# Kernel tuning notes

Hardware: AMD Instinct MI355X
Metric: run time of the kernel (lower is better)

## Reference

```python
import jax, jax.numpy as jnp
import numpy as np

ORIG_H, ORIG_W = 256, 192
NUM_HEADS = 8
KSZ, SIGMA = 5, 2.0

def _gauss_kernel(dtype):
    off = jnp.arange(KSZ, dtype=jnp.float32) - (KSZ // 2)
    g = jnp.exp(-(off[:, None] ** 2 + off[None, :] ** 2) / (2.0 * SIGMA ** 2))
    return (g / g.sum()).astype(dtype)

def _gauss_pool(fm, kpts):
    # fm: (B,C,H,W), kpts: (B,N,2) [x,y] in original image coords -> (B,N,C)
    B, C, H, W = fm.shape
    scale = jnp.array([W / ORIG_W, H / ORIG_H], dtype=fm.dtype)
    rk = kpts * scale  # resized to feature-map coords
    off = jnp.arange(KSZ) - KSZ // 2
    ix = jnp.clip(jnp.round(rk[..., 0]).astype(jnp.int32)[..., None] + off, 0, W - 1)  # (B,N,K)
    iy = jnp.clip(jnp.round(rk[..., 1]).astype(jnp.int32)[..., None] + off, 0, H - 1)  # (B,N,K)
    fmT = fm.transpose(0, 2, 3, 1)  # (B,H,W,C)
    gather = jax.vmap(lambda f, yy, xx: f[yy[:, :, None], xx[:, None, :]])(fmT, iy, ix)  # (B,N,K,K,C)
    return jnp.einsum('bnyxc,yx->bnc', gather, _gauss_kernel(fm.dtype))

def _ln(x, g, b):
    m = x.mean(-1, keepdims=True)
    v = x.var(-1, keepdims=True)
    return (x - m) / jnp.sqrt(v + 1e-5) * g + b

def _gated_attn(x, wqkv, bqkv, wg, bg, wo, bo):
    # x: (M,S,C); headwise-gated multi-head self-attention
    M, S, C = x.shape
    H = NUM_HEADS
    d = C // H
    q, k, v = jnp.split(x @ wqkv + bqkv, 3, axis=-1)
    q = q.reshape(M, S, H, d); k = k.reshape(M, S, H, d); v = v.reshape(M, S, H, d)
    att = jax.nn.softmax(jnp.einsum('mshd,mthd->mhst', q, k) * (1.0 / np.sqrt(d)), axis=-1)
    o = jnp.einsum('mhst,mthd->mshd', att, v)
    gate = jax.nn.sigmoid(x @ wg + bg)  # (M,S,H) headwise gate
    o = (o * gate[..., None]).reshape(M, S, C)
    return o @ wo + bo

def _fuse(kf, ms, proj_p, attn_p):
    B, N, C = kf.shape
    meta = jnp.broadcast_to(ms[None], (B, N, C))
    w1, b1, g, beta, w2, b2 = proj_p
    h = _ln(jnp.concatenate([kf, meta], axis=-1) @ w1 + b1, g, beta)
    projected = jax.nn.relu(h) @ w2 + b2
    stacked = jnp.stack([kf, meta], axis=2).reshape(B * N, 2, C)  # (B*N,2,C)
    attended = _gated_attn(stacked, *attn_p).reshape(B, N, 2, C)
    return attended.mean(axis=2) + projected

def setup_inputs() -> dict:
    key = jax.random.key(0)
    ks = iter(jax.random.split(key, 48))
    B, N = 32, 17
    dims = [256, 512]
    inp = {}
    inp['fm0'] = jax.random.normal(next(ks), (B, 256, 96, 72), jnp.float32)
    inp['fm1'] = jax.random.normal(next(ks), (B, 512, 48, 36), jnp.float32)
    u = jax.random.uniform(next(ks), (B, N, 2), jnp.float32)
    inp['keypoints'] = u * jnp.array([ORIG_W - 1.0, ORIG_H - 1.0], jnp.float32)
    for i, C in enumerate(dims):
        s = 1.0 / np.sqrt(C)
        inp[f'ms{i}'] = jax.random.normal(next(ks), (N, C), jnp.float32) * s
        inp[f'p{i}_w1'] = jax.random.normal(next(ks), (2 * C, C), jnp.float32) * (1.0 / np.sqrt(2 * C))
        inp[f'p{i}_b1'] = jnp.zeros((C,), jnp.float32)
        inp[f'p{i}_g'] = jnp.ones((C,), jnp.float32)
        inp[f'p{i}_beta'] = jnp.zeros((C,), jnp.float32)
        inp[f'p{i}_w2'] = jax.random.normal(next(ks), (C, C), jnp.float32) * s
        inp[f'p{i}_b2'] = jnp.zeros((C,), jnp.float32)
        inp[f'a{i}_wqkv'] = jax.random.normal(next(ks), (C, 3 * C), jnp.float32) * s
        inp[f'a{i}_bqkv'] = jnp.zeros((3 * C,), jnp.float32)
        inp[f'a{i}_wg'] = jax.random.normal(next(ks), (C, NUM_HEADS), jnp.float32) * s
        inp[f'a{i}_bg'] = jnp.zeros((NUM_HEADS,), jnp.float32)
        inp[f'a{i}_wo'] = jax.random.normal(next(ks), (C, C), jnp.float32) * s
        inp[f'a{i}_bo'] = jnp.zeros((C,), jnp.float32)
    return inp

def reference(fm0, fm1, keypoints,
              ms0, p0_w1, p0_b1, p0_g, p0_beta, p0_w2, p0_b2,
              a0_wqkv, a0_bqkv, a0_wg, a0_bg, a0_wo, a0_bo,
              ms1, p1_w1, p1_b1, p1_g, p1_beta, p1_w2, p1_b2,
              a1_wqkv, a1_bqkv, a1_wg, a1_bg, a1_wo, a1_bo):
    kf0 = _gauss_pool(fm0, keypoints)
    f0 = _fuse(kf0, ms0, (p0_w1, p0_b1, p0_g, p0_beta, p0_w2, p0_b2),
               (a0_wqkv, a0_bqkv, a0_wg, a0_bg, a0_wo, a0_bo))
    kf1 = _gauss_pool(fm1, keypoints)
    f1 = _fuse(kf1, ms1, (p1_w1, p1_b1, p1_g, p1_beta, p1_w2, p1_b2),
               (a1_wqkv, a1_bqkv, a1_wg, a1_bg, a1_wo, a1_bo))
    return (f0, f1)
```

## Files before the change

### kernel.cpp

```cpp
#include <hip/hip_runtime.h>
#include <math.h>

#define NKPT 17
#define BATCH 32
#define MROW 544
#define MPAD 576

typedef unsigned short u16;
typedef _Float16 half8 __attribute__((ext_vector_type(8)));
typedef float f32x4 __attribute__((ext_vector_type(4)));

__device__ __forceinline__ u16 f2h(float f) {
    _Float16 h = (_Float16)f;
    u16 u; __builtin_memcpy(&u, &h, 2); return u;
}
__device__ __forceinline__ float h2f(u16 u) {
    _Float16 h; __builtin_memcpy(&h, &u, 2); return (float)h;
}

struct GDp {
    const u16* A; const u16* BT; const float* bias; u16* dst;
    int lda, ldd, K, N, ntiles, sk;
};
struct GPp { GDp d[4]; int blk0[5]; int nd; };

__global__ __launch_bounds__(256) void gemm_part(GPp P)
{
    __shared__ u16 sA[2][64][72];
    __shared__ u16 sB[2][64][72];
    int bid = blockIdx.x, gi = 0;
    while (gi + 1 < P.nd && bid >= P.blk0[gi + 1]) ++gi;
    const GDp g = P.d[gi];
    int local = bid - P.blk0[gi];
    const int nspan = g.ntiles * g.sk;
    const int mt = local / nspan;
    int rem = local - mt * nspan;
    const int nt = rem / g.sk;
    const int s  = rem - nt * g.sk;
    const int m0 = mt * 64, n0 = nt * 64;
    const int Kseg = g.K / g.sk;
    const int kbase = s * Kseg;

    const int t = threadIdx.x;
    const int l = t & 63, w = t >> 6, wr = w >> 1, wc = w & 1;
    const int row = t >> 2, kc = (t & 3) << 4;

    f32x4 acc[2][2];
    #pragma unroll
    for (int i = 0; i < 2; ++i)
        #pragma unroll
        for (int j = 0; j < 2; ++j) { f32x4 z = {0.f,0.f,0.f,0.f}; acc[i][j] = z; }

    const u16* ap = g.A  + (size_t)(m0 + row) * g.lda + kbase + kc;
    const u16* bp = g.BT + (size_t)(n0 + row) * g.K   + kbase + kc;
    uint4 ra0 = *(const uint4*)ap, ra1 = *(const uint4*)(ap + 8);
    uint4 rb0 = *(const uint4*)bp, rb1 = *(const uint4*)(bp + 8);
    *(uint4*)&sA[0][row][kc] = ra0; *(uint4*)&sA[0][row][kc + 8] = ra1;
    *(uint4*)&sB[0][row][kc] = rb0; *(uint4*)&sB[0][row][kc + 8] = rb1;
    __syncthreads();

    int cur = 0;
    for (int k0 = 0; k0 < Kseg; k0 += 64) {
        const bool nxt = (k0 + 64 < Kseg);
        if (nxt) {
            ra0 = *(const uint4*)(ap + k0 + 64); ra1 = *(const uint4*)(ap + k0 + 72);
            rb0 = *(const uint4*)(bp + k0 + 64); rb1 = *(const uint4*)(bp + k0 + 72);
        }
        #pragma unroll
        for (int ks = 0; ks < 64; ks += 32) {
            const int koff = ks + (l >> 4) * 8;
            half8 af0 = *(const half8*)&sA[cur][wr * 32 +      (l & 15)][koff];
            half8 af1 = *(const half8*)&sA[cur][wr * 32 + 16 + (l & 15)][koff];
            half8 bf0 = *(const half8*)&sB[cur][wc * 32 +      (l & 15)][koff];
            half8 bf1 = *(const half8*)&sB[cur][wc * 32 + 16 + (l & 15)][koff];
            acc[0][0] = __builtin_amdgcn_mfma_f32_16x16x32_f16(af0, bf0, acc[0][0], 0, 0, 0);
            acc[0][1] = __builtin_amdgcn_mfma_f32_16x16x32_f16(af0, bf1, acc[0][1], 0, 0, 0);
            acc[1][0] = __builtin_amdgcn_mfma_f32_16x16x32_f16(af1, bf0, acc[1][0], 0, 0, 0);
            acc[1][1] = __builtin_amdgcn_mfma_f32_16x16x32_f16(af1, bf1, acc[1][1], 0, 0, 0);
        }
        if (nxt) {
            int nb = cur ^ 1;
            *(uint4*)&sA[nb][row][kc] = ra0; *(uint4*)&sA[nb][row][kc + 8] = ra1;
            *(uint4*)&sB[nb][row][kc] = rb0; *(uint4*)&sB[nb][row][kc + 8] = rb1;
            __syncthreads();
            cur = nb;
        }
    }

    u16* dbase = g.dst + (size_t)s * MPAD * g.ldd;
    #pragma unroll
    for (int i = 0; i < 2; ++i) {
        #pragma unroll
        for (int j = 0; j < 2; ++j) {
            int col = n0 + wc * 32 + j * 16 + (l & 15);
            float bv = (s == 0) ? g.bias[col] : 0.f;
            #pragma unroll
            for (int rr = 0; rr < 4; ++rr) {
                int m = m0 + wr * 32 + i * 16 + (l >> 4) * 4 + rr;
                dbase[(size_t)m * g.ldd + col] = f2h(acc[i][j][rr] + bv);
            }
        }
    }
}

struct GDo {
    const u16* A; const u16* BT; const float* bias; float* dst;
    int lda, ldd, K, N, mstore, ntiles;
};
struct GPo { GDo d[2]; int blk0[3]; int nd; };

__global__ __launch_bounds__(256) void gemm_out(GPo P)
{
    __shared__ u16 sA[2][32][72];
    __shared__ u16 sB[2][64][72];
    int bid = blockIdx.x, gi = 0;
    while (gi + 1 < P.nd && bid >= P.blk0[gi + 1]) ++gi;
    const GDo g = P.d[gi];
    int local = bid - P.blk0[gi];
    const int mt = local / g.ntiles, nt = local % g.ntiles;
    const int m0 = mt * 32, n0 = nt * 64;

    const int t = threadIdx.x;
    const int l = t & 63, w = t >> 6, wr = w >> 1, wc = w & 1;
    const int rowA = t >> 3, kcA = (t & 7) << 3;
    const int rowB = t >> 2, kcB = (t & 3) << 4;

    f32x4 acc[2];
    { f32x4 z = {0.f,0.f,0.f,0.f}; acc[0] = z; acc[1] = z; }

    const u16* ap = g.A  + (size_t)(m0 + rowA) * g.lda + kcA;
    const u16* bp = g.BT + (size_t)(n0 + rowB) * g.K   + kcB;
    uint4 ra  = *(const uint4*)ap;
    uint4 rb0 = *(const uint4*)bp, rb1 = *(const uint4*)(bp + 8);
    *(uint4*)&sA[0][rowA][kcA] = ra;
    *(uint4*)&sB[0][rowB][kcB] = rb0; *(uint4*)&sB[0][rowB][kcB + 8] = rb1;
    __syncthreads();

    int cur = 0;
    for (int k0 = 0; k0 < g.K; k0 += 64) {
        const bool nxt = (k0 + 64 < g.K);
        if (nxt) {
            ra  = *(const uint4*)(ap + k0 + 64);
            rb0 = *(const uint4*)(bp + k0 + 64); rb1 = *(const uint4*)(bp + k0 + 72);
        }
        #pragma unroll
        for (int ks = 0; ks < 64; ks += 32) {
            const int koff = ks + (l >> 4) * 8;
            half8 af  = *(const half8*)&sA[cur][wr * 16 + (l & 15)][koff];
            half8 bf0 = *(const half8*)&sB[cur][wc * 32 +      (l & 15)][koff];
            half8 bf1 = *(const half8*)&sB[cur][wc * 32 + 16 + (l & 15)][koff];
            acc[0] = __builtin_amdgcn_mfma_f32_16x16x32_f16(af, bf0, acc[0], 0, 0, 0);
            acc[1] = __builtin_amdgcn_mfma_f32_16x16x32_f16(af, bf1, acc[1], 0, 0, 0);
        }
        if (nxt) {
            int nb = cur ^ 1;
            *(uint4*)&sA[nb][rowA][kcA] = ra;
            *(uint4*)&sB[nb][rowB][kcB] = rb0; *(uint4*)&sB[nb][rowB][kcB + 8] = rb1;
            __syncthreads();
            cur = nb;
        }
    }

    #pragma unroll
    for (int j = 0; j < 2; ++j) {
        int col = n0 + wc * 32 + j * 16 + (l & 15);
        float bv = g.bias[col];
        #pragma unroll
        for (int rr = 0; rr < 4; ++rr) {
            int m = m0 + wr * 16 + (l >> 4) * 4 + rr;
            if (m < g.mstore)
                g.dst[(size_t)m * g.ldd + col] = acc[j][rr] + bv;
        }
    }
}

struct TD { const float* src; u16* dst; int K, N, ld, koff, blk0; };
struct PrepP {
    const float *fm0, *fm1, *kp, *ms0, *ms1;
    const float *wg0, *bg0, *wg1, *bg1;
    const float *b2_1, *bo_1, *b2_0, *bo_0;
    u16 *A1h_0, *A1h_1;
    float *gout0, *gout1;
    float *bsum1, *bsum0;
    TD td[8];
};

__device__ void gates_from_sx(const float* sx, int C, const float* wg,
                              const float* bg, float* gout8)
{
    int t = threadIdx.x;
    int h = t >> 5, e = t & 31;
    float a = 0.f;
    for (int c = e; c < C; c += 32) a += sx[c] * wg[c * 8 + h];
    a += __shfl_xor(a, 16, 32); a += __shfl_xor(a, 8, 32);
    a += __shfl_xor(a, 4, 32);  a += __shfl_xor(a, 2, 32);
    a += __shfl_xor(a, 1, 32);
    if (e == 0) gout8[h] = 1.0f / (1.0f + expf(-(a + bg[h])));
}

template<int C, int H, int W>
__device__ void pool_row(int b, int n, const float* fm, const float* kp,
                         const float* ms, u16* A1h, const float* wg,
                         const float* bg, float* gout, float* sx)
{
    const int t = threadIdx.x;
    const int e = t & 31, grp = t >> 5;
    float kx = kp[(b * NKPT + n) * 2 + 0];
    float ky = kp[(b * NKPT + n) * 2 + 1];
    int cx = (int)rintf(kx * ((float)W / 192.0f));
    int cy = (int)rintf(ky * ((float)H / 256.0f));
    int dy = e / 5, dx = e % 5;
    float wgt = 0.f; int off = 0;
    if (e < 25) {
        int iy = min(max(cy + dy - 2, 0), H - 1);
        int ix = min(max(cx + dx - 2, 0), W - 1);
        off = iy * W + ix;
        wgt = expf(-(float)((dy - 2) * (dy - 2) + (dx - 2) * (dx - 2)) / 8.0f);
    }
    float ws_ = wgt;
    ws_ += __shfl_xor(ws_, 16, 32); ws_ += __shfl_xor(ws_, 8, 32);
    ws_ += __shfl_xor(ws_, 4, 32);  ws_ += __shfl_xor(ws_, 2, 32);
    ws_ += __shfl_xor(ws_, 1, 32);
    const float inv = 1.0f / ws_;

    const size_t plane = (size_t)H * W;
    const float* pf = fm + ((size_t)b * C + grp) * plane + off;
    #pragma unroll 4
    for (int c0 = grp; c0 < C; c0 += 8, pf += 8 * plane) {
        float v = 0.f;
        if (e < 25) v = wgt * (*pf);
        v += __shfl_xor(v, 16, 32); v += __shfl_xor(v, 8, 32);
        v += __shfl_xor(v, 4, 32);  v += __shfl_xor(v, 2, 32);
        v += __shfl_xor(v, 1, 32);
        if (e == 0) sx[c0] = v * inv;
    }
    __syncthreads();
    u16* rowh = A1h + (size_t)(b * NKPT + n) * (2 * C);
    for (int c = t; c < C; c += 256) {
        rowh[c] = f2h(sx[c]);
        rowh[C + c] = f2h(ms[n * C + c]);
    }
    gates_from_sx(sx, C, wg, bg, gout + (size_t)(b * NKPT + n) * 8);
}

template<int C>
__device__ void meta_row(int n, const float* ms, u16* A1h, const float* wg,
                         const float* bg, float* gout, float* sx)
{
    const int t = threadIdx.x;
    u16* rowh = A1h + (size_t)(MROW + n) * (2 * C);
    for (int c = t; c < C; c += 256) {
        float v = ms[n * C + c];
        sx[c] = v;
        rowh[c] = f2h(v);
        rowh[C + c] = 0;
    }
    __syncthreads();
    gates_from_sx(sx, C, wg, bg, gout + (size_t)(MROW + n) * 8);
}

__device__ void wtrans_tile(const TD& d, int u, float* sT)
{
    const int ntx = d.N >> 6;
    const int tk = u / ntx, tn = u % ntx;
    const int k0 = tk << 6, n0 = tn << 6;
    const int t = threadIdx.x;
    {
        int r = t >> 2, cq = (t & 3) << 4;
        const float* sp = d.src + (size_t)(k0 + r) * d.N + n0 + cq;
        #pragma unroll
        for (int i = 0; i < 4; ++i) {
            float4 v = *(const float4*)(sp + 4 * i);
            sT[r * 65 + cq + 4 * i + 0] = v.x;
            sT[r * 65 + cq + 4 * i + 1] = v.y;
            sT[r * 65 + cq + 4 * i + 2] = v.z;
            sT[r * 65 + cq + 4 * i + 3] = v.w;
        }
    }
    __syncthreads();
    {
        int nn = t >> 2, kq = (t & 3) << 4;
        u16 hv[16] __attribute__((aligned(16)));
        #pragma unroll
        for (int i = 0; i < 16; ++i) hv[i] = f2h(sT[(kq + i) * 65 + nn]);
        u16* dp = d.dst + (size_t)(n0 + nn) * d.ld + d.koff + k0 + kq;
        *reinterpret_cast<uint4*>(dp) = *reinterpret_cast<uint4*>(&hv[0]);
        *reinterpret_cast<uint4*>(dp + 8) = *reinterpret_cast<uint4*>(&hv[8]);
    }
}

__global__ __launch_bounds__(256) void k1_prep(PrepP P)
{
    __shared__ float ps[64 * 65];
    int bid = blockIdx.x;
    if (bid < 1088) {
        if (bid < 544) pool_row<512, 48, 36>(bid / NKPT, bid % NKPT, P.fm1, P.kp, P.ms1, P.A1h_1, P.wg1, P.bg1, P.gout1, ps);
        else { int r = bid - 544; pool_row<256, 96, 72>(r / NKPT, r % NKPT, P.fm0, P.kp, P.ms0, P.A1h_0, P.wg0, P.bg0, P.gout0, ps); }
    } else if (bid < 1122) {
        int u = bid - 1088;
        if (u < NKPT) meta_row<512>(u, P.ms1, P.A1h_1, P.wg1, P.bg1, P.gout1, ps);
        else          meta_row<256>(u - NKPT, P.ms0, P.A1h_0, P.wg0, P.bg0, P.gout0, ps);
    } else if (bid < 1682) {
        int u = bid - 1122, i = 0;
        while (i + 1 < 8 && u >= P.td[i + 1].blk0) ++i;
        wtrans_tile(P.td[i], u - P.td[i].blk0, ps);
    } else {
        int t = threadIdx.x;
        for (int c = t; c < 512; c += 256) P.bsum1[c] = P.b2_1[c] + P.bo_1[c];
        for (int c = t; c < 256; c += 256) P.bsum0[c] = P.b2_0[c] + P.bo_0[c];
    }
}

template<int C>
__device__ void attn_row(int r, const u16* qkvp, const float* gout,
                         u16* A4, float* sred)
{
    constexpr int D = C / 8;
    constexpr int TC = 3 * C;
    const size_t PS = (size_t)MPAD * TC;
    const int t = threadIdx.x;
    const int n = r % NKPT;
    const size_t rb = (size_t)r * TC;
    const size_t mb = (size_t)(MROW + n) * TC;
    {
        int dot = t >> 3, sub = t & 7;
        int p = dot >> 3, h = dot & 7;
        size_t qb = ((p & 2) ? mb : rb) + h * D + sub * (D / 8);
        size_t kb = ((p & 1) ? mb : rb) + C + h * D + sub * (D / 8);
        float a = 0.f;
        #pragma unroll
        for (int i = 0; i < D / 8; ++i) {
            float qv = h2f(qkvp[qb + i]) + h2f(qkvp[qb + i + PS]);
            float kv = h2f(qkvp[kb + i]) + h2f(qkvp[kb + i + PS]);
            a += qv * kv;
        }
        a += __shfl_xor(a, 4, 8); a += __shfl_xor(a, 2, 8); a += __shfl_xor(a, 1, 8);
        if (sub == 0) sred[dot] = a;
    }
    if (t >= 32 && t < 40) sred[32 + (t - 32)] = gout[(size_t)r * 8 + (t - 32)];
    else if (t >= 40 && t < 48) sred[32 + (t - 32)] = gout[(size_t)(MROW + n) * 8 + (t - 40)];
    __syncthreads();
    if (t < 8) {
        int h = t;
        float scale = (float)(1.0 / sqrt((double)D));
        float c0 = 0.f, c1 = 0.f;
        #pragma unroll
        for (int s = 0; s < 2; ++s) {
            float a0 = sred[(2 * s) * 8 + h] * scale;
            float a1 = sred[(2 * s + 1) * 8 + h] * scale;
            float mx = fmaxf(a0, a1);
            float e0 = expf(a0 - mx), e1 = expf(a1 - mx);
            float inv = 1.0f / (e0 + e1);
            float gt = sred[32 + s * 8 + h];
            c0 += e0 * inv * gt;
            c1 += e1 * inv * gt;
        }
        sred[48 + h] = 0.5f * c0;
        sred[56 + h] = 0.5f * c1;
    }
    __syncthreads();
    for (int c = t; c < C; c += 256) {
        int h = c / D;
        float v0 = h2f(qkvp[rb + 2 * C + c]) + h2f(qkvp[rb + 2 * C + c + PS]);
        float v1 = h2f(qkvp[mb + 2 * C + c]) + h2f(qkvp[mb + 2 * C + c + PS]);
        A4[(size_t)r * (2 * C) + C + c] = f2h(sred[48 + h] * v0 + sred[56 + h] * v1);
    }
}

struct RP {
    const u16 *hp1, *hp0;
    u16 *A4_1, *A4_0;
    const float *g1, *be1, *g0, *be0;
    const u16 *qkvp1, *qkvp0;
    const float *gout1, *gout0;
};
__global__ __launch_bounds__(256) void k3_rowops(RP P)
{
    __shared__ float sh[64];
    int bid = blockIdx.x;
    if (bid < 1088) {
        int lvl1 = bid < 544;
        int r = lvl1 ? bid : bid - 544;
        int C = lvl1 ? 512 : 256;
        const u16* hp = lvl1 ? P.hp1 : P.hp0;
        const size_t PSh = (size_t)MPAD * C;
        u16* A4 = (lvl1 ? P.A4_1 : P.A4_0) + (size_t)r * (2 * C);
        const float* gg = lvl1 ? P.g1 : P.g0;
        const float* bb = lvl1 ? P.be1 : P.be0;
        int t = threadIdx.x;
        int nc = C >> 8;
        float v[2] = {0.f, 0.f};
        float s1 = 0.f, s2 = 0.f;
        for (int i = 0; i < nc; ++i) {
            size_t idx = (size_t)r * C + t + (i << 8);
            float x = h2f(hp[idx]) + h2f(hp[idx + PSh]);
            v[i] = x; s1 += x; s2 += x * x;
        }
        #pragma unroll
        for (int o = 32; o > 0; o >>= 1) { s1 += __shfl_down(s1, o); s2 += __shfl_down(s2, o); }
        int lane = t & 63, wv = t >> 6;
        if (lane == 0) { sh[wv * 2] = s1; sh[wv * 2 + 1] = s2; }
        __syncthreads();
        if (t == 0) {
            float a = 0.f, b = 0.f;
            #pragma unroll
            for (int q = 0; q < 4; ++q) { a += sh[q * 2]; b += sh[q * 2 + 1]; }
            float m = a / (float)C;
            float var = b / (float)C - m * m;
            sh[8] = m; sh[9] = 1.0f / sqrtf(var + 1e-5f);
        }
        __syncthreads();
        float m = sh[8], rs = sh[9];
        for (int i = 0; i < nc; ++i) {
            int c = t + (i << 8);
            float x = (v[i] - m) * rs * gg[c] + bb[c];
            A4[c] = f2h(fmaxf(x, 0.f));
        }
    } else {
        int a = bid - 1088;
        if (a < 544) attn_row<512>(a, P.qkvp1, P.gout1, P.A4_1, sh);
        else         attn_row<256>(a - 544, P.qkvp0, P.gout0, P.A4_0, sh);
    }
}

template<int C, int H, int W>
__global__ __launch_bounds__(C) void fb_level(
    const float* __restrict__ fm, const float* __restrict__ kp,
    const float* __restrict__ ms, const float* __restrict__ w1,
    const float* __restrict__ b1, const float* __restrict__ gvec,
    const float* __restrict__ beta, const float* __restrict__ w2,
    const float* __restrict__ b2, const float* __restrict__ wqkv,
    const float* __restrict__ bqkv, const float* __restrict__ wg,
    const float* __restrict__ bg, const float* __restrict__ wo,
    const float* __restrict__ bo, float* __restrict__ out)
{
    constexpr int D = C / 8;
    constexpr int NW = C / 64;
    __shared__ float x0[C], x1[C], hbuf[C];
    __shared__ float q0[C], k0[C], v0[C], q1[C], k1[C], v1[C];
    __shared__ float om[C];
    __shared__ float gw[25];
    __shared__ float gwsum_inv;
    __shared__ float redA[NW], redB[NW];
    __shared__ float stats[2];
    __shared__ float gates[2][8];
    __shared__ float att[2][2][8];
    const int j = threadIdx.x;
    const int blk = blockIdx.x;
    const int b = blk / NKPT, n = blk % NKPT;
    if (j < 25) { int dy = j / 5 - 2, dx = j % 5 - 2; gw[j] = expf(-(float)(dy*dy+dx*dx) / 8.0f); }
    __syncthreads();
    if (j == 0) { float s = 0.f; for (int t2 = 0; t2 < 25; ++t2) s += gw[t2]; gwsum_inv = 1.0f / s; }
    float kx = kp[(b * NKPT + n) * 2 + 0];
    float ky = kp[(b * NKPT + n) * 2 + 1];
    int cx = (int)rintf(kx * ((float)W / 192.0f));
    int cy = (int)rintf(ky * ((float)H / 256.0f));
    int ix[5], iy[5];
    #pragma unroll
    for (int t2 = 0; t2 < 5; ++t2) {
        ix[t2] = min(max(cx + t2 - 2, 0), W - 1);
        iy[t2] = min(max(cy + t2 - 2, 0), H - 1);
    }
    __syncthreads();
    {
        const float* fmb = fm + ((size_t)b * C + j) * (H * W);
        float acc = 0.f;
        #pragma unroll
        for (int yy = 0; yy < 5; ++yy) {
            const float* row = fmb + iy[yy] * W;
            #pragma unroll
            for (int xx = 0; xx < 5; ++xx) acc += gw[yy * 5 + xx] * row[ix[xx]];
        }
        x0[j] = acc * gwsum_inv;
        x1[j] = ms[n * C + j];
    }
    __syncthreads();
    float hacc = b1[j];
    for (int i = 0; i < C; ++i) hacc += x0[i] * w1[i * C + j];
    for (int i = 0; i < C; ++i) hacc += x1[i] * w1[(C + i) * C + j];
    {
        float s1 = hacc, s2 = hacc * hacc;
        #pragma unroll
        for (int o = 32; o > 0; o >>= 1) { s1 += __shfl_down(s1, o); s2 += __shfl_down(s2, o); }
        int lane = j & 63, wid = j >> 6;
        if (lane == 0) { redA[wid] = s1; redB[wid] = s2; }
        __syncthreads();
        if (j == 0) {
            float t1 = 0.f, t2 = 0.f;
            for (int w = 0; w < NW; ++w) { t1 += redA[w]; t2 += redB[w]; }
            float m = t1 / (float)C, v = t2 / (float)C - m * m;
            stats[0] = m; stats[1] = 1.0f / sqrtf(v + 1e-5f);
        }
        __syncthreads();
    }
    hbuf[j] = fmaxf((hacc - stats[0]) * stats[1] * gvec[j] + beta[j], 0.f);
    __syncthreads();
    float pj = b2[j];
    for (int i = 0; i < C; ++i) pj += hbuf[i] * w2[i * C + j];
    {
        float aq0 = bqkv[j], ak0 = bqkv[C + j], av0 = bqkv[2 * C + j];
        float aq1 = aq0, ak1 = ak0, av1 = av0;
        for (int i = 0; i < C; ++i) {
            float xi0 = x0[i], xi1 = x1[i];
            const float* wr = wqkv + (size_t)i * (3 * C);
            float wq = wr[j], wk = wr[C + j], wv = wr[2 * C + j];
            aq0 += xi0 * wq; aq1 += xi1 * wq;
            ak0 += xi0 * wk; ak1 += xi1 * wk;
            av0 += xi0 * wv; av1 += xi1 * wv;
        }
        q0[j] = aq0; k0[j] = ak0; v0[j] = av0;
        q1[j] = aq1; k1[j] = ak1; v1[j] = av1;
    }
    __syncthreads();
    if (j < 16) {
        int s = j >> 3, hh = j & 7;
        const float* xs = s ? x1 : x0;
        float a = bg[hh];
        for (int i = 0; i < C; ++i) a += xs[i] * wg[i * 8 + hh];
        gates[s][hh] = 1.0f / (1.0f + expf(-a));
    }
    if (j < 32) {
        int hh = j >> 2, st = j & 3;
        const float* qs = (st & 2) ? q1 : q0;
        const float* kt = (st & 1) ? k1 : k0;
        float a = 0.f;
        for (int i = hh * D; i < (hh + 1) * D; ++i) a += qs[i] * kt[i];
        att[(st >> 1)][st & 1][hh] = a;
    }
    __syncthreads();
    if (j < 16) {
        int s = j >> 3, hh = j & 7;
        const float inv = 1.0f / sqrtf((float)D);
        float a0 = att[s][0][hh] * inv, a1 = att[s][1][hh] * inv;
        float mx = fmaxf(a0, a1);
        float e0 = expf(a0 - mx), e1 = expf(a1 - mx);
        float den = e0 + e1;
        att[s][0][hh] = e0 / den; att[s][1][hh] = e1 / den;
    }
    __syncthreads();
    {
        int hh = j / D;
        float o0 = (att[0][0][hh] * v0[j] + att[0][1][hh] * v1[j]) * gates[0][hh];
        float o1 = (att[1][0][hh] * v0[j] + att[1][1][hh] * v1[j]) * gates[1][hh];
        om[j] = 0.5f * (o0 + o1);
    }
    __syncthreads();
    float oacc = bo[j];
    for (int i = 0; i < C; ++i) oacc += om[i] * wo[i * C + j];
    out[((size_t)b * NKPT + n) * C + j] = oacc + pj;
}

extern "C" void kernel_launch(void* const* d_in, const int* in_sizes, int n_in,
                              void* d_out, int out_size, void* d_ws, size_t ws_size,
                              hipStream_t stream) {
    (void)in_sizes; (void)n_in; (void)out_size;
    const float* fm0  = (const float*)d_in[0];
    const float* fm1  = (const float*)d_in[1];
    const float* kp   = (const float*)d_in[2];
    const float* ms0     = (const float*)d_in[3];
    const float* p0_w1   = (const float*)d_in[4];
    const float* p0_b1   = (const float*)d_in[5];
    const float* p0_g    = (const float*)d_in[6];
    const float* p0_beta = (const float*)d_in[7];
    const float* p0_w2   = (const float*)d_in[8];
    const float* p0_b2   = (const float*)d_in[9];
    const float* a0_wqkv = (const float*)d_in[10];
    const float* a0_bqkv = (const float*)d_in[11];
    const float* a0_wg   = (const float*)d_in[12];
    const float* a0_bg   = (const float*)d_in[13];
    const float* a0_wo   = (const float*)d_in[14];
    const float* a0_bo   = (const float*)d_in[15];
    const float* ms1     = (const float*)d_in[16];
    const float* p1_w1   = (const float*)d_in[17];
    const float* p1_b1   = (const float*)d_in[18];
    const float* p1_g    = (const float*)d_in[19];
    const float* p1_beta = (const float*)d_in[20];
    const float* p1_w2   = (const float*)d_in[21];
    const float* p1_b2   = (const float*)d_in[22];
    const float* a1_wqkv = (const float*)d_in[23];
    const float* a1_bqkv = (const float*)d_in[24];
    const float* a1_wg   = (const float*)d_in[25];
    const float* a1_bg   = (const float*)d_in[26];
    const float* a1_wo   = (const float*)d_in[27];
    const float* a1_bo   = (const float*)d_in[28];

    float* out0 = (float*)d_out;
    float* out1 = (float*)d_out + (size_t)MROW * 256;

    const size_t WS_NEED = 15400000;
    if (ws_size < WS_NEED || d_ws == nullptr) {
        fb_level<256, 96, 72><<<MROW, 256, 0, stream>>>(
            fm0, kp, ms0, p0_w1, p0_b1, p0_g, p0_beta, p0_w2, p0_b2,
            a0_wqkv, a0_bqkv, a0_wg, a0_bg, a0_wo, a0_bo, out0);
        fb_level<512, 48, 36><<<MROW, 512, 0, stream>>>(
            fm1, kp, ms1, p1_w1, p1_b1, p1_g, p1_beta, p1_w2, p1_b2,
            a1_wqkv, a1_bqkv, a1_wg, a1_bg, a1_wo, a1_bo, out1);
        return;
    }

    char* cur = (char*)d_ws;
    auto alloc = [&](size_t bytes) { char* p = cur; cur += (bytes + 255) & ~(size_t)255; return p; };
    u16* A1h_1 = (u16*)alloc((size_t)MPAD * 1024 * 2);
    u16* A1h_0 = (u16*)alloc((size_t)MPAD * 512 * 2);
    u16* hp_1  = (u16*)alloc((size_t)2 * MPAD * 512 * 2);
    u16* hp_0  = (u16*)alloc((size_t)2 * MPAD * 256 * 2);
    u16* qkvp_1 = (u16*)alloc((size_t)2 * MPAD * 1536 * 2);
    u16* qkvp_0 = (u16*)alloc((size_t)2 * MPAD * 768 * 2);
    u16* A4_1  = (u16*)alloc((size_t)MPAD * 1024 * 2);
    u16* A4_0  = (u16*)alloc((size_t)MPAD * 512 * 2);
    u16* w1T_1   = (u16*)alloc((size_t)512 * 1024 * 2);
    u16* wqkvT_1 = (u16*)alloc((size_t)1536 * 512 * 2);
    u16* w24T_1  = (u16*)alloc((size_t)512 * 1024 * 2);
    u16* w1T_0   = (u16*)alloc((size_t)256 * 512 * 2);
    u16* wqkvT_0 = (u16*)alloc((size_t)768 * 256 * 2);
    u16* w24T_0  = (u16*)alloc((size_t)256 * 512 * 2);
    float* gout1 = (float*)alloc((size_t)(MROW + NKPT) * 8 * 4);
    float* gout0 = (float*)alloc((size_t)(MROW + NKPT) * 8 * 4);
    float* bsum1 = (float*)alloc(512 * 4);
    float* bsum0 = (float*)alloc(256 * 4);

    PrepP pp;
    pp.fm0 = fm0; pp.fm1 = fm1; pp.kp = kp; pp.ms0 = ms0; pp.ms1 = ms1;
    pp.wg0 = a0_wg; pp.bg0 = a0_bg; pp.wg1 = a1_wg; pp.bg1 = a1_bg;
    pp.b2_1 = p1_b2; pp.bo_1 = a1_bo; pp.b2_0 = p0_b2; pp.bo_0 = a0_bo;
    pp.A1h_0 = A1h_0; pp.A1h_1 = A1h_1;
    pp.gout0 = gout0; pp.gout1 = gout1;
    pp.bsum1 = bsum1; pp.bsum0 = bsum0;
    int tcum = 0;
    auto setTD = [&](int i, const float* src, u16* dst, int K, int N, int ld, int koff) {
        pp.td[i].src = src; pp.td[i].dst = dst; pp.td[i].K = K; pp.td[i].N = N;
        pp.td[i].ld = ld; pp.td[i].koff = koff;
        pp.td[i].blk0 = tcum; tcum += (K / 64) * (N / 64);
    };
    setTD(0, p1_w1,   w1T_1,   1024, 512,  1024, 0);
    setTD(1, a1_wqkv, wqkvT_1, 512,  1536, 512,  0);
    setTD(2, p1_w2,   w24T_1,  512,  512,  1024, 0);
    setTD(3, a1_wo,   w24T_1,  512,  512,  1024, 512);
    setTD(4, p0_w1,   w1T_0,   512,  256,  512,  0);
    setTD(5, a0_wqkv, wqkvT_0, 256,  768,  256,  0);
    setTD(6, p0_w2,   w24T_0,  256,  256,  512,  0);
    setTD(7, a0_wo,   w24T_0,  256,  256,  512,  256);
    k1_prep<<<1683, 256, 0, stream>>>(pp);

    GPp g2; g2.nd = 4;
    g2.d[0] = { A1h_1, w1T_1,   p1_b1,   hp_1,   1024, 512,  1024, 512,  8,  2 };
    g2.d[1] = { A1h_1, wqkvT_1, a1_bqkv, qkvp_1, 1024, 1536, 512,  1536, 24, 2 };
    g2.d[2] = { A1h_0, w1T_0,   p0_b1,   hp_0,   512,  256,  512,  256,  4,  2 };
    g2.d[3] = { A1h_0, wqkvT_0, a0_bqkv, qkvp_0, 512,  768,  256,  768,  12, 2 };
    g2.blk0[0] = 0;
    for (int i = 0; i < 4; ++i) g2.blk0[i + 1] = g2.blk0[i] + 9 * g2.d[i].ntiles * g2.d[i].sk;
    gemm_part<<<g2.blk0[4], 256, 0, stream>>>(g2);

    RP rp;
    rp.hp1 = hp_1; rp.hp0 = hp_0; rp.A4_1 = A4_1; rp.A4_0 = A4_0;
    rp.g1 = p1_g; rp.be1 = p1_beta; rp.g0 = p0_g; rp.be0 = p0_beta;
    rp.qkvp1 = qkvp_1; rp.qkvp0 = qkvp_0;
    rp.gout1 = gout1; rp.gout0 = gout0;
    k3_rowops<<<2176, 256, 0, stream>>>(rp);

    GPo g4; g4.nd = 2;
    g4.d[0] = { A4_1, w24T_1, bsum1, out1, 1024, 512, 1024, 512, MROW, 8 };
    g4.d[1] = { A4_0, w24T_0, bsum0, out0, 512,  256, 512,  256, MROW, 4 };
    g4.blk0[0] = 0;
    for (int i = 0; i < 2; ++i) g4.blk0[i + 1] = g4.blk0[i] + 18 * g4.d[i].ntiles;
    gemm_out<<<g4.blk0[2], 256, 0, stream>>>(g4);
}
```

Before: 82.30 us.

## Shrink output GEMM N-tile, merge LN and attention rows, nontemporal pooling loads

The output GEMM N-tile drops from 64 to 32 columns. Each warp now computes one 16x16 MFMA tile instead of two, which doubles the block count so more blocks are available to fill the GPU. The row-ops kernel now runs layernorm and attention for the same row in one block, halving the grid and removing separate launches of half-idle blocks. The feature-map pooling loads now use nontemporal hints to avoid polluting the cache. The costs are less reuse per block in the GEMM and longer per-block work in the row-ops kernel.

```diff
diff --git a/kernel.cpp b/kernel.cpp
--- a/kernel.cpp
+++ b/kernel.cpp
@@ -112,64 +112,60 @@
 __global__ __launch_bounds__(256) void gemm_out(GPo P)
 {
     __shared__ u16 sA[2][32][72];
-    __shared__ u16 sB[2][64][72];
+    __shared__ u16 sB[2][32][72];
     int bid = blockIdx.x, gi = 0;
     while (gi + 1 < P.nd && bid >= P.blk0[gi + 1]) ++gi;
     const GDo g = P.d[gi];
     int local = bid - P.blk0[gi];
     const int mt = local / g.ntiles, nt = local % g.ntiles;
-    const int m0 = mt * 32, n0 = nt * 64;
+    const int m0 = mt * 32, n0 = nt * 32;
 
     const int t = threadIdx.x;
     const int l = t & 63, w = t >> 6, wr = w >> 1, wc = w & 1;
-    const int rowA = t >> 3, kcA = (t & 7) << 3;
-    const int rowB = t >> 2, kcB = (t & 3) << 4;
-
-    f32x4 acc[2];
-    { f32x4 z = {0.f,0.f,0.f,0.f}; acc[0] = z; acc[1] = z; }
-
-    const u16* ap = g.A  + (size_t)(m0 + rowA) * g.lda + kcA;
-    const u16* bp = g.BT + (size_t)(n0 + rowB) * g.K   + kcB;
-    uint4 ra  = *(const uint4*)ap;
-    uint4 rb0 = *(const uint4*)bp, rb1 = *(const uint4*)(bp + 8);
-    *(uint4*)&sA[0][rowA][kcA] = ra;
-    *(uint4*)&sB[0][rowB][kcB] = rb0; *(uint4*)&sB[0][rowB][kcB + 8] = rb1;
+    const int rowS = t >> 3, kcS = (t & 7) << 3;
+
+    f32x4 acc;
+    { f32x4 z = {0.f,0.f,0.f,0.f}; acc = z; }
+
+    const u16* ap = g.A  + (size_t)(m0 + rowS) * g.lda + kcS;
+    const u16* bp = g.BT + (size_t)(n0 + rowS) * g.K   + kcS;
+    uint4 ra = *(const uint4*)ap;
+    uint4 rb = *(const uint4*)bp;
+    *(uint4*)&sA[0][rowS][kcS] = ra;
+    *(uint4*)&sB[0][rowS][kcS] = rb;
     __syncthreads();
 
     int cur = 0;
     for (int k0 = 0; k0 < g.K; k0 += 64) {
         const bool nxt = (k0 + 64 < g.K);
         if (nxt) {
-            ra  = *(const uint4*)(ap + k0 + 64);
-            rb0 = *(const uint4*)(bp + k0 + 64); rb1 = *(const uint4*)(bp + k0 + 72);
+            ra = *(const uint4*)(ap + k0 + 64);
+            rb = *(const uint4*)(bp + k0 + 64);
         }
         #pragma unroll
         for (int ks = 0; ks < 64; ks += 32) {
             const int koff = ks + (l >> 4) * 8;
-            half8 af  = *(const half8*)&sA[cur][wr * 16 + (l & 15)][koff];
-            half8 bf0 = *(const half8*)&sB[cur][wc * 32 +      (l & 15)][koff];
-            half8 bf1 = *(const half8*)&sB[cur][wc * 32 + 16 + (l & 15)][koff];
-            acc[0] = __builtin_amdgcn_mfma_f32_16x16x32_f16(af, bf0, acc[0], 0, 0, 0);
-            acc[1] = __builtin_amdgcn_mfma_f32_16x16x32_f16(af, bf1, acc[1], 0, 0, 0);
+            half8 af = *(const half8*)&sA[cur][wr * 16 + (l & 15)][koff];
+            half8 bf = *(const half8*)&sB[cur][wc * 16 + (l & 15)][koff];
+            acc = __builtin_amdgcn_mfma_f32_16x16x32_f16(af, bf, acc, 0, 0, 0);
         }
         if (nxt) {
             int nb = cur ^ 1;
-            *(uint4*)&sA[nb][rowA][kcA] = ra;
-            *(uint4*)&sB[nb][rowB][kcB] = rb0; *(uint4*)&sB[nb][rowB][kcB + 8] = rb1;
+            *(uint4*)&sA[nb][rowS][kcS] = ra;
+            *(uint4*)&sB[nb][rowS][kcS] = rb;
             __syncthreads();
             cur = nb;
         }
     }
 
-    #pragma unroll
-    for (int j = 0; j < 2; ++j) {
-        int col = n0 + wc * 32 + j * 16 + (l & 15);
+    {
+        int col = n0 + wc * 16 + (l & 15);
         float bv = g.bias[col];
         #pragma unroll
         for (int rr = 0; rr < 4; ++rr) {
             int m = m0 + wr * 16 + (l >> 4) * 4 + rr;
             if (m < g.mstore)
-                g.dst[(size_t)m * g.ldd + col] = acc[j][rr] + bv;
+                g.dst[(size_t)m * g.ldd + col] = acc[rr] + bv;
         }
     }
 }
@@ -228,7 +224,7 @@
     #pragma unroll 4
     for (int c0 = grp; c0 < C; c0 += 8, pf += 8 * plane) {
         float v = 0.f;
-        if (e < 25) v = wgt * (*pf);
+        if (e < 25) v = wgt * __builtin_nontemporal_load(pf);
         v += __shfl_xor(v, 16, 32); v += __shfl_xor(v, 8, 32);
         v += __shfl_xor(v, 4, 32);  v += __shfl_xor(v, 2, 32);
         v += __shfl_xor(v, 1, 32);
@@ -312,8 +308,44 @@
 }
 
 template<int C>
+__device__ void ln_row(int r, const u16* hp, const float* gg, const float* bb,
+                       u16* A4row, float* sh)
+{
+    const size_t PSh = (size_t)MPAD * C;
+    const int t = threadIdx.x;
+    const int nc = C >> 8;
+    float v[2] = {0.f, 0.f};
+    float s1 = 0.f, s2 = 0.f;
+    for (int i = 0; i < nc; ++i) {
+        size_t idx = (size_t)r * C + t + (i << 8);
+        float x = h2f(hp[idx]) + h2f(hp[idx + PSh]);
+        v[i] = x; s1 += x; s2 += x * x;
+    }
+    #pragma unroll
+    for (int o = 32; o > 0; o >>= 1) { s1 += __shfl_down(s1, o); s2 += __shfl_down(s2, o); }
+    int lane = t & 63, wv = t >> 6;
+    if (lane == 0) { sh[wv * 2] = s1; sh[wv * 2 + 1] = s2; }
+    __syncthreads();
+    if (t == 0) {
+        float a = 0.f, b = 0.f;
+        #pragma unroll
+        for (int q = 0; q < 4; ++q) { a += sh[q * 2]; b += sh[q * 2 + 1]; }
+        float m = a / (float)C;
+        float var = b / (float)C - m * m;
+        sh[8] = m; sh[9] = 1.0f / sqrtf(var + 1e-5f);
+    }
+    __syncthreads();
+    float m = sh[8], rs = sh[9];
+    for (int i = 0; i < nc; ++i) {
+        int c = t + (i << 8);
+        float x = (v[i] - m) * rs * gg[c] + bb[c];
+        A4row[c] = f2h(fmaxf(x, 0.f));
+    }
+}
+
+template<int C>
 __device__ void attn_row(int r, const u16* qkvp, const float* gout,
-                         u16* A4, float* sred)
+                         u16* A4row, float* sred)
 {
     constexpr int D = C / 8;
     constexpr int TC = 3 * C;
@@ -363,7 +395,7 @@
         int h = c / D;
         float v0 = h2f(qkvp[rb + 2 * C + c]) + h2f(qkvp[rb + 2 * C + c + PS]);
         float v1 = h2f(qkvp[mb + 2 * C + c]) + h2f(qkvp[mb + 2 * C + c + PS]);
-        A4[(size_t)r * (2 * C) + C + c] = f2h(sred[48 + h] * v0 + sred[56 + h] * v1);
+        A4row[C + c] = f2h(sred[48 + h] * v0 + sred[56 + h] * v1);
     }
 }
 
@@ -378,48 +410,18 @@
 {
     __shared__ float sh[64];
     int bid = blockIdx.x;
-    if (bid < 1088) {
-        int lvl1 = bid < 544;
-        int r = lvl1 ? bid : bid - 544;
-        int C = lvl1 ? 512 : 256;
-        const u16* hp = lvl1 ? P.hp1 : P.hp0;
-        const size_t PSh = (size_t)MPAD * C;
-        u16* A4 = (lvl1 ? P.A4_1 : P.A4_0) + (size_t)r * (2 * C);
-        const float* gg = lvl1 ? P.g1 : P.g0;
-        const float* bb = lvl1 ? P.be1 : P.be0;
-        int t = threadIdx.x;
-        int nc = C >> 8;
-        float v[2] = {0.f, 0.f};
-        float s1 = 0.f, s2 = 0.f;
-        for (int i = 0; i < nc; ++i) {
-            size_t idx = (size_t)r * C + t + (i << 8);
-            float x = h2f(hp[idx]) + h2f(hp[idx + PSh]);
-            v[i] = x; s1 += x; s2 += x * x;
-        }
-        #pragma unroll
-        for (int o = 32; o > 0; o >>= 1) { s1 += __shfl_down(s1, o); s2 += __shfl_down(s2, o); }
-        int lane = t & 63, wv = t >> 6;
-        if (lane == 0) { sh[wv * 2] = s1; sh[wv * 2 + 1] = s2; }
+    int lvl1 = bid < 544;
+    int r = lvl1 ? bid : bid - 544;
+    if (lvl1) {
+        u16* A4row = P.A4_1 + (size_t)r * 1024;
+        ln_row<512>(r, P.hp1, P.g1, P.be1, A4row, sh);
         __syncthreads();
-        if (t == 0) {
-            float a = 0.f, b = 0.f;
-            #pragma unroll
-            for (int q = 0; q < 4; ++q) { a += sh[q * 2]; b += sh[q * 2 + 1]; }
-            float m = a / (float)C;
-            float var = b / (float)C - m * m;
-            sh[8] = m; sh[9] = 1.0f / sqrtf(var + 1e-5f);
-        }
+        attn_row<512>(r, P.qkvp1, P.gout1, A4row, sh);
+    } else {
+        u16* A4row = P.A4_0 + (size_t)r * 512;
+        ln_row<256>(r, P.hp0, P.g0, P.be0, A4row, sh);
         __syncthreads();
-        float m = sh[8], rs = sh[9];
-        for (int i = 0; i < nc; ++i) {
-            int c = t + (i << 8);
-            float x = (v[i] - m) * rs * gg[c] + bb[c];
-            A4[c] = f2h(fmaxf(x, 0.f));
-        }
-    } else {
-        int a = bid - 1088;
-        if (a < 544) attn_row<512>(a, P.qkvp1, P.gout1, P.A4_1, sh);
-        else         attn_row<256>(a - 544, P.qkvp0, P.gout0, P.A4_0, sh);
+        attn_row<256>(r, P.qkvp0, P.gout0, A4row, sh);
     }
 }
 
@@ -656,11 +658,11 @@
     rp.g1 = p1_g; rp.be1 = p1_beta; rp.g0 = p0_g; rp.be0 = p0_beta;
     rp.qkvp1 = qkvp_1; rp.qkvp0 = qkvp_0;
     rp.gout1 = gout1; rp.gout0 = gout0;
-    k3_rowops<<<2176, 256, 0, stream>>>(rp);
+    k3_rowops<<<1088, 256, 0, stream>>>(rp);
 
     GPo g4; g4.nd = 2;
-    g4.d[0] = { A4_1, w24T_1, bsum1, out1, 1024, 512, 1024, 512, MROW, 8 };
-    g4.d[1] = { A4_0, w24T_0, bsum0, out0, 512,  256, 512,  256, MROW, 4 };
+    g4.d[0] = { A4_1, w24T_1, bsum1, out1, 1024, 512, 1024, 512, MROW, 16 };
+    g4.d[1] = { A4_0, w24T_0, bsum0, out0, 512,  256, 512,  256, MROW, 8 };
     g4.blk0[0] = 0;
     for (int i = 0; i < 2; ++i) g4.blk0[i + 1] = g4.blk0[i] + 18 * g4.d[i].ntiles;
     gemm_out<<<g4.blk0[2], 256, 0, stream>>>(g4);
```

After: 98.35 us. 19.5% more time.
